# Kernel optimization log

Measured on AMD Instinct MI355X. Metric: run time of the kernel, lower is better.

The kernel has to match this reference:

```python
import jax, jax.numpy as jnp
import numpy as np

N_NODES = 50000
N_EDGES = 800000
IN_CH = 128
HID = 256
OUT_CH = 10
N_GRAPHS = 64


def setup_inputs() -> dict:
    key = jax.random.key(0)
    ks = jax.random.split(key, 16)
    s = 0.02
    inp = {
        "x": jax.random.normal(ks[0], (N_NODES, IN_CH), dtype=jnp.float32),
        "edge_index": jax.random.randint(ks[1], (2, N_EDGES), 0, N_NODES, dtype=jnp.int64),
        "batch": jnp.sort(jax.random.randint(ks[2], (N_NODES,), 0, N_GRAPHS, dtype=jnp.int64)),
        # SAGEConv params: out = lin_l(mean_agg) + lin_r(x_root); lin_l has bias, lin_r does not (PyG default)
        "W1l": jax.random.normal(ks[3], (HID, IN_CH), dtype=jnp.float32) * s,
        "b1": jnp.zeros((HID,), jnp.float32),
        "W1r": jax.random.normal(ks[4], (HID, IN_CH), dtype=jnp.float32) * s,
        "W2l": jax.random.normal(ks[5], (HID, HID), dtype=jnp.float32) * s,
        "b2": jnp.zeros((HID,), jnp.float32),
        "W2r": jax.random.normal(ks[6], (HID, HID), dtype=jnp.float32) * s,
        "W3l": jax.random.normal(ks[7], (HID, HID), dtype=jnp.float32) * s,
        "b3": jnp.zeros((HID,), jnp.float32),
        "W3r": jax.random.normal(ks[8], (HID, HID), dtype=jnp.float32) * s,
        "lin1_W": jax.random.normal(ks[9], (HID // 2, HID), dtype=jnp.float32) * s,
        "lin1_b": jnp.zeros((HID // 2,), jnp.float32),
        "lin2_W": jax.random.normal(ks[10], (OUT_CH, HID // 2), dtype=jnp.float32) * s,
        "lin2_b": jnp.zeros((OUT_CH,), jnp.float32),
    }
    return inp


def _sage_conv(x, src, dst, Wl, bl, Wr):
    # mean-aggregate neighbor features at destination nodes
    msg_sum = jax.ops.segment_sum(x[src], dst, num_segments=N_NODES)  # [N, d]
    deg = jax.ops.segment_sum(jnp.ones((src.shape[0],), x.dtype), dst, num_segments=N_NODES)
    agg = msg_sum / jnp.maximum(deg, 1.0)[:, None]
    return agg @ Wl.T + bl + x @ Wr.T


def reference(x, edge_index, batch, W1l, b1, W1r, W2l, b2, W2r, W3l, b3, W3r,
              lin1_W, lin1_b, lin2_W, lin2_b):
    src, dst = edge_index[0], edge_index[1]
    h = jax.nn.relu(_sage_conv(x, src, dst, W1l, b1, W1r))
    h = jax.nn.relu(_sage_conv(h, src, dst, W2l, b2, W2r))
    h = jax.nn.relu(_sage_conv(h, src, dst, W3l, b3, W3r))
    # global_mean_pool over batch vector
    pooled_sum = jax.ops.segment_sum(h, batch, num_segments=N_GRAPHS)  # [G, HID]
    counts = jax.ops.segment_sum(jnp.ones((h.shape[0],), h.dtype), batch, num_segments=N_GRAPHS)
    g = pooled_sum / jnp.maximum(counts, 1.0)[:, None]
    g = jax.nn.relu(g @ lin1_W.T + lin1_b)
    # dropout is identity in eval mode
    return g @ lin2_W.T + lin2_b
```

## Files before the change

kernel.cpp:

```cpp
#include <hip/hip_runtime.h>
#include <hip/hip_bf16.h>


#define HID 256
typedef unsigned short ushort_t;
typedef __bf16 bf16x8 __attribute__((ext_vector_type(8)));
typedef float  f32x4  __attribute__((ext_vector_type(4)));
typedef float  f32x2  __attribute__((ext_vector_type(2)));

__device__ __forceinline__ unsigned short f2bf(float f) {
    unsigned int u = __float_as_uint(f);
    unsigned int r = (u + 0x7fffu + ((u >> 16) & 1u)) >> 16;
    return (unsigned short)r;
}
__device__ __forceinline__ float bflo(unsigned int u) { return __uint_as_float(u << 16); }
__device__ __forceinline__ float bfhi(unsigned int u) { return __uint_as_float(u & 0xffff0000u); }
__device__ __forceinline__ unsigned int packbf(float a, float b) {
    return (unsigned int)f2bf(a) | ((unsigned int)f2bf(b) << 16);
}
__device__ __forceinline__ void gld16(const void* g, void* l) {
    __builtin_amdgcn_global_load_lds(
        (const __attribute__((address_space(1))) unsigned int*)g,
        (__attribute__((address_space(3))) unsigned int*)l, 16, 0, 0);
}
__device__ __forceinline__ void fma8(float* a, float w, const uint4 v) {
    a[0] = fmaf(w, bflo(v.x), a[0]); a[1] = fmaf(w, bfhi(v.x), a[1]);
    a[2] = fmaf(w, bflo(v.y), a[2]); a[3] = fmaf(w, bfhi(v.y), a[3]);
    a[4] = fmaf(w, bflo(v.z), a[4]); a[5] = fmaf(w, bfhi(v.z), a[5]);
    a[6] = fmaf(w, bflo(v.w), a[6]); a[7] = fmaf(w, bfhi(v.w), a[7]);
}
__device__ __forceinline__ void fma8_f8(float* a, float w, const uint2 v) {
    const f32x2 c01 = __builtin_amdgcn_cvt_pk_f32_fp8(v.x, false);
    const f32x2 c23 = __builtin_amdgcn_cvt_pk_f32_fp8(v.x, true);
    const f32x2 c45 = __builtin_amdgcn_cvt_pk_f32_fp8(v.y, false);
    const f32x2 c67 = __builtin_amdgcn_cvt_pk_f32_fp8(v.y, true);
    a[0] = fmaf(w, c01.x, a[0]); a[1] = fmaf(w, c01.y, a[1]);
    a[2] = fmaf(w, c23.x, a[2]); a[3] = fmaf(w, c23.y, a[3]);
    a[4] = fmaf(w, c45.x, a[4]); a[5] = fmaf(w, c45.y, a[5]);
    a[6] = fmaf(w, c67.x, a[6]); a[7] = fmaf(w, c67.y, a[7]);
}
__device__ __forceinline__ void acc8(float* a, const uint4 v) {
    a[0] += bflo(v.x); a[1] += bfhi(v.x);
    a[2] += bflo(v.y); a[3] += bfhi(v.y);
    a[4] += bflo(v.z); a[5] += bfhi(v.z);
    a[6] += bflo(v.w); a[7] += bfhi(v.w);
}
__device__ __forceinline__ int4 load4idx(const int* __restrict__ csr, int pbase, int e1m1) {
    int4 r;
    r.x = csr[min(pbase + 0, e1m1)];
    r.y = csr[min(pbase + 1, e1m1)];
    r.z = csr[min(pbase + 2, e1m1)];
    r.w = csr[min(pbase + 3, e1m1)];
    return r;
}

#define NBUCK 256
#define NPB_BUCK 196
#define BCAP 4096

__global__ __launch_bounds__(256)
void cvt_kernel(const float* __restrict__ x, ushort_t* __restrict__ xb, int nx4,
                const float* __restrict__ W1l, const float* __restrict__ W1r,
                const float* __restrict__ W2l, const float* __restrict__ W2r,
                const float* __restrict__ W3l, const float* __restrict__ W3r,
                ushort_t* __restrict__ wdst, int s1, int s2,
                int* __restrict__ bcursor) {
    const int t = blockIdx.x * 256 + threadIdx.x;
    if (t < NBUCK) bcursor[t] = 0;
    if (t < nx4) {
        const int i = t * 4;
        const float4 v = *(const float4*)(x + i);
        *(uint2*)(xb + i) = make_uint2(packbf(v.x, v.y), packbf(v.z, v.w));
        return;
    }
    int off = t - nx4;
    const int total = 2 * s1 + 4 * s2;
    if (off >= total) return;
    const int i = off;
    const float* src;
    if (off < s1) src = W1l;
    else if ((off -= s1) < s1) src = W1r;
    else if ((off -= s1) < s2) src = W2l;
    else if ((off -= s2) < s2) src = W2r;
    else if ((off -= s2) < s2) src = W3l;
    else { off -= s2; src = W3r; }
    wdst[i] = f2bf(src[off]);
}

__global__ __launch_bounds__(256)
void binA_kernel(const int* __restrict__ src, const int* __restrict__ dst,
                 int* __restrict__ bcursor, unsigned int* __restrict__ staging, int E) {
    __shared__ int hist[NBUCK];
    __shared__ int wbase[NBUCK];
    const int tid = threadIdx.x;
    hist[tid] = 0;
    __syncthreads();
    const int i0 = blockIdx.x * 2048;
    int d8[8], s8[8], b8[8];
    #pragma unroll
    for (int j = 0; j < 8; ++j) {
        const int i = i0 + j * 256 + tid;
        if (i < E) {
            d8[j] = dst[i];
            s8[j] = src[i];
            b8[j] = d8[j] / NPB_BUCK;
            atomicAdd(&hist[b8[j]], 1);
        } else b8[j] = -1;
    }
    __syncthreads();
    {
        const int b = tid;
        const int cnt = hist[b];
        int wb = 0;
        if (cnt > 0) wb = atomicAdd(&bcursor[b], cnt);
        wbase[b] = b * BCAP + wb;
        hist[b] = 0;
    }
    __syncthreads();
    #pragma unroll
    for (int j = 0; j < 8; ++j) {
        if (b8[j] >= 0) {
            const int pos = wbase[b8[j]] + atomicAdd(&hist[b8[j]], 1);
            if (pos < (b8[j] + 1) * BCAP)
                staging[pos] = ((unsigned int)(d8[j] - b8[j] * NPB_BUCK) << 16) | (unsigned int)s8[j];
        }
    }
}

__global__ __launch_bounds__(256)
void binB_kernel(const unsigned int* __restrict__ staging, const int* __restrict__ bcursor,
                 int* __restrict__ csr, int* __restrict__ offsets, int nn, int E) {
    __shared__ unsigned int sedge[BCAP];
    __shared__ int cnt[NBUCK];
    __shared__ int bsum[4];
    __shared__ int wt[4];
    const int b = blockIdx.x, tid = threadIdx.x;
    const int lane = tid & 63, wid = tid >> 6;

    int part = (tid < b) ? bcursor[tid] : 0;
    #pragma unroll
    for (int d = 1; d < 64; d <<= 1) part += __shfl_xor(part, d, 64);
    if (lane == 0) bsum[wid] = part;
    const int mycnt = min(bcursor[b], BCAP);
    __syncthreads();
    const int base = bsum[0] + bsum[1] + bsum[2] + bsum[3];

    for (int i = tid; i < mycnt; i += 256) sedge[i] = staging[b * BCAP + i];
    cnt[tid] = 0;
    __syncthreads();
    for (int i = tid; i < mycnt; i += 256) atomicAdd(&cnt[sedge[i] >> 16], 1);
    __syncthreads();

    const int v = cnt[tid];
    int incl = v;
    #pragma unroll
    for (int d = 1; d < 64; d <<= 1) {
        int t = __shfl_up(incl, d, 64);
        if (lane >= d) incl += t;
    }
    if (lane == 63) wt[wid] = incl;
    __syncthreads();
    int wb = 0;
    #pragma unroll
    for (int w = 0; w < 4; ++w) { int t = wt[w]; if (w < wid) wb += t; }
    const int excl = wb + incl - v;

    const int node = b * NPB_BUCK + tid;
    if (tid < NPB_BUCK && node < nn) offsets[node] = base + excl;
    if (b == NBUCK - 1 && tid == 0) offsets[nn] = E;
    __syncthreads();
    cnt[tid] = excl;
    __syncthreads();

    for (int i = tid; i < mycnt; i += 256) {
        const unsigned int e = sedge[i];
        const int p = atomicAdd(&cnt[e >> 16], 1);
        csr[base + p] = (int)(e & 0xFFFFu);
    }
}

template <int C>
__global__ __launch_bounds__(256)
void agg_kernel(const ushort_t* __restrict__ h, const int* __restrict__ offsets,
                const int* __restrict__ csr, ushort_t* __restrict__ out, int nn) {
    constexpr int CL = C / 8;
    constexpr int EW = 64 / CL;
    constexpr int RPE = 4 * EW;
    const int node = (blockIdx.x * 256 + threadIdx.x) >> 6;
    if (node >= nn) return;
    const int lane = threadIdx.x & 63;
    const int cl = lane & (CL - 1);
    const int eo = lane / CL;
    const int e0 = offsets[node], e1 = offsets[node + 1];
    const int deg = e1 - e0;
    const int rounds = (deg + RPE - 1) / RPE;
    const int e1m1 = max(e1 - 1, 0);
    float a[8] = {0.f, 0.f, 0.f, 0.f, 0.f, 0.f, 0.f, 0.f};
    int pb = e0 + eo * 4;
    if (rounds > 0) {
        int4 idx = load4idx(csr, pb, e1m1);
        for (int r2 = 0; r2 < rounds; ++r2) {
            const int4 cur = idx;
            const int pcur = pb;
            pb += RPE;
            if (r2 + 1 < rounds) idx = load4idx(csr, pb, e1m1);
            const uint4 v0 = *(const uint4*)(h + (size_t)cur.x * C + cl * 8);
            const uint4 v1 = *(const uint4*)(h + (size_t)cur.y * C + cl * 8);
            const uint4 v2 = *(const uint4*)(h + (size_t)cur.z * C + cl * 8);
            const uint4 v3 = *(const uint4*)(h + (size_t)cur.w * C + cl * 8);
            fma8(a, (pcur + 0 < e1) ? 1.f : 0.f, v0);
            fma8(a, (pcur + 1 < e1) ? 1.f : 0.f, v1);
            fma8(a, (pcur + 2 < e1) ? 1.f : 0.f, v2);
            fma8(a, (pcur + 3 < e1) ? 1.f : 0.f, v3);
        }
    }
    #pragma unroll
    for (int d = CL; d < 64; d <<= 1)
        #pragma unroll
        for (int r = 0; r < 8; ++r) a[r] += __shfl_xor(a[r], d, 64);
    if (eo == 0) {
        const float inv = 1.0f / fmaxf((float)deg, 1.0f);
        uint4 o;
        o.x = packbf(a[0] * inv, a[1] * inv);
        o.y = packbf(a[2] * inv, a[3] * inv);
        o.z = packbf(a[4] * inv, a[5] * inv);
        o.w = packbf(a[6] * inv, a[7] * inv);
        *(uint4*)(out + (size_t)node * C + cl * 8) = o;
    }
}

__global__ __launch_bounds__(256)
void agg8_kernel(const unsigned char* __restrict__ h8, const int* __restrict__ offsets,
                 const int* __restrict__ csr, ushort_t* __restrict__ out, int nn) {
    const int node = (blockIdx.x * 256 + threadIdx.x) >> 6;
    if (node >= nn) return;
    const int lane = threadIdx.x & 63;
    const int cl = lane & 31;
    const int eo = lane >> 5;
    const int e0 = offsets[node], e1 = offsets[node + 1];
    const int deg = e1 - e0;
    const int rounds = (deg + 7) / 8;
    const int e1m1 = max(e1 - 1, 0);
    float a[8] = {0.f, 0.f, 0.f, 0.f, 0.f, 0.f, 0.f, 0.f};
    int pb = e0 + eo * 4;
    if (rounds > 0) {
        int4 idx = load4idx(csr, pb, e1m1);
        for (int r2 = 0; r2 < rounds; ++r2) {
            const int4 cur = idx;
            const int pcur = pb;
            pb += 8;
            if (r2 + 1 < rounds) idx = load4idx(csr, pb, e1m1);
            const uint2 v0 = *(const uint2*)(h8 + (size_t)cur.x * 256 + cl * 8);
            const uint2 v1 = *(const uint2*)(h8 + (size_t)cur.y * 256 + cl * 8);
            const uint2 v2 = *(const uint2*)(h8 + (size_t)cur.z * 256 + cl * 8);
            const uint2 v3 = *(const uint2*)(h8 + (size_t)cur.w * 256 + cl * 8);
            fma8_f8(a, (pcur + 0 < e1) ? 1.f : 0.f, v0);
            fma8_f8(a, (pcur + 1 < e1) ? 1.f : 0.f, v1);
            fma8_f8(a, (pcur + 2 < e1) ? 1.f : 0.f, v2);
            fma8_f8(a, (pcur + 3 < e1) ? 1.f : 0.f, v3);
        }
    }
    #pragma unroll
    for (int r = 0; r < 8; ++r) a[r] += __shfl_xor(a[r], 32, 64);
    if (eo == 0) {
        const float inv = 1.0f / fmaxf((float)deg, 1.0f);
        uint4 o;
        o.x = packbf(a[0] * inv, a[1] * inv);
        o.y = packbf(a[2] * inv, a[3] * inv);
        o.z = packbf(a[4] * inv, a[5] * inv);
        o.w = packbf(a[6] * inv, a[7] * inv);
        *(uint4*)(out + (size_t)node * 256 + cl * 8) = o;
    }
}

template <int K, bool W8>
__global__ __launch_bounds__(256, 2)
void gemm2_mfma(const ushort_t* __restrict__ A1, const ushort_t* __restrict__ A2,
                const ushort_t* __restrict__ W1, const ushort_t* __restrict__ W2,
                const float* __restrict__ bias, ushort_t* __restrict__ Cout,
                unsigned char* __restrict__ H8, int M) {
    __shared__ ushort_t As[2 * 128 * 64];
    __shared__ ushort_t Bs[2 * 128 * 64];
    const int tid = threadIdx.x;
    const int row0 = blockIdx.x * 128, col0 = blockIdx.y * 128;
    const int wave = tid >> 6, lane = tid & 63;
    const int wm = (wave & 1) * 64, wn = (wave >> 1) * 64;
    const int l15 = lane & 15, quad = lane >> 4;
    constexpr int NCH = K / 128;

    f32x4 acc[4][4] = {};

    #pragma unroll
    for (int phase = 0; phase < 2; ++phase) {
        const ushort_t* __restrict__ A = phase ? A2 : A1;
        const ushort_t* __restrict__ W = phase ? W2 : W1;
        for (int kc = 0; kc < NCH; ++kc) {
            const int kt = kc * 128;
            __syncthreads();
            #pragma unroll
            for (int p = 0; p < 8; ++p) {
                const int slot = p * 256 + tid;
                const int g = slot >> 10;
                const int r = (slot >> 3) & 127;
                const int c = slot & 7;
                const int cg = c ^ (r & 7);
                int ar = row0 + r; if (ar >= M) ar = M - 1;
                gld16(A + (size_t)ar * K + kt + g * 64 + cg * 8, &As[slot * 8]);
            }
            #pragma unroll
            for (int p = 0; p < 8; ++p) {
                const int slot = p * 256 + tid;
                const int g = slot >> 10;
                const int r = (slot >> 3) & 127;
                const int c = slot & 7;
                const int cg = c ^ (r & 7);
                gld16(W + (size_t)(col0 + r) * K + kt + g * 64 + cg * 8, &Bs[slot * 8]);
            }
            __syncthreads();
            #pragma unroll
            for (int g = 0; g < 2; ++g) {
                #pragma unroll
                for (int ks = 0; ks < 2; ++ks) {
                    const int kq = ks * 4 + quad;
                    bf16x8 af[4], bfv[4];
                    #pragma unroll
                    for (int i = 0; i < 4; ++i) {
                        const int r = wm + i * 16 + l15;
                        const int cl = kq ^ (r & 7);
                        af[i] = *(const bf16x8*)&As[g * 8192 + r * 64 + cl * 8];
                    }
                    #pragma unroll
                    for (int j = 0; j < 4; ++j) {
                        const int r = wn + j * 16 + l15;
                        const int cl = kq ^ (r & 7);
                        bfv[j] = *(const bf16x8*)&Bs[g * 8192 + r * 64 + cl * 8];
                    }
                    #pragma unroll
                    for (int i = 0; i < 4; ++i)
                        #pragma unroll
                        for (int j = 0; j < 4; ++j)
                            acc[i][j] = __builtin_amdgcn_mfma_f32_16x16x32_bf16(
                                af[i], bfv[j], acc[i][j], 0, 0, 0);
                }
            }
        }
    }

    #pragma unroll
    for (int i = 0; i < 4; ++i) {
        const int mbase = row0 + wm + i * 16 + quad * 4;
        #pragma unroll
        for (int j = 0; j < 4; ++j) {
            const int n = col0 + wn + j * 16 + l15;
            const float b = bias[n];
            #pragma unroll
            for (int reg = 0; reg < 4; ++reg) {
                const int mr = mbase + reg;
                const float v = fmaxf(acc[i][j][reg] + b, 0.f);
                const float vp = __shfl_xor(v, 1, 64);
                if (!(l15 & 1) && mr < M)
                    *(unsigned int*)(Cout + (size_t)mr * 256 + n) = packbf(v, vp);
                if (W8) {
                    const int p2 = __builtin_amdgcn_cvt_pk_fp8_f32(v, vp, 0, false);
                    const int q2 = __shfl_xor(p2, 2, 64);
                    if ((l15 & 3) == 0 && mr < M)
                        *(unsigned int*)(H8 + (size_t)mr * 256 + n) =
                            ((unsigned int)p2 & 0xFFFFu) | ((unsigned int)q2 << 16);
                }
            }
        }
    }
}

__global__ __launch_bounds__(256)
void pool_mlp_kernel(const ushort_t* __restrict__ h, const int* __restrict__ batch, int nn,
                     const float* __restrict__ lin1W, const float* __restrict__ lin1b,
                     const float* __restrict__ lin2W, const float* __restrict__ lin2b,
                     float* __restrict__ out) {
    const int g = blockIdx.x;
    const int tid = threadIdx.x;
    int lo = 0, hi = nn;
    while (lo < hi) { int mid = (lo + hi) >> 1; if (batch[mid] < g) lo = mid + 1; else hi = mid; }
    const int s = lo;
    hi = nn;
    while (lo < hi) { int mid = (lo + hi) >> 1; if (batch[mid] < g + 1) lo = mid + 1; else hi = mid; }
    const int e = lo;

    const int cl = tid & 31, rg = tid >> 5;
    float a[8] = {0.f, 0.f, 0.f, 0.f, 0.f, 0.f, 0.f, 0.f};
    for (int n = s + rg; n < e; n += 8) {
        const uint4 v = *(const uint4*)(h + (size_t)n * 256 + cl * 8);
        acc8(a, v);
    }
    __shared__ float red[8][256];
    #pragma unroll
    for (int r = 0; r < 8; ++r) red[rg][cl * 8 + r] = a[r];
    __syncthreads();
    __shared__ float meanv[256];
    float ssum = 0.f;
    #pragma unroll
    for (int r = 0; r < 8; ++r) ssum += red[r][tid];
    meanv[tid] = ssum / fmaxf((float)(e - s), 1.0f);
    __syncthreads();
    __shared__ float g1[128];
    if (tid < 128) {
        float acc = lin1b[tid];
        #pragma unroll 4
        for (int k = 0; k < 256; k += 4) {
            const float4 w = *(const float4*)(lin1W + tid * 256 + k);
            acc += meanv[k] * w.x + meanv[k + 1] * w.y + meanv[k + 2] * w.z + meanv[k + 3] * w.w;
        }
        g1[tid] = fmaxf(acc, 0.f);
    }
    __syncthreads();
    if (tid < 10) {
        float o = lin2b[tid];
        #pragma unroll 4
        for (int k = 0; k < 128; k += 4) {
            const float4 w = *(const float4*)(lin2W + tid * 128 + k);
            o += g1[k] * w.x + g1[k + 1] * w.y + g1[k + 2] * w.z + g1[k + 3] * w.w;
        }
        out[g * 10 + tid] = o;
    }
}

extern "C" void kernel_launch(void* const* d_in, const int* in_sizes, int n_in,
                              void* d_out, int out_size, void* d_ws, size_t ws_size,
                              hipStream_t stream) {
    const float* x     = (const float*)d_in[0];
    const int*   eidx  = (const int*)d_in[1];
    const int*   batch = (const int*)d_in[2];
    const float* W1l = (const float*)d_in[3];
    const float* b1  = (const float*)d_in[4];
    const float* W1r = (const float*)d_in[5];
    const float* W2l = (const float*)d_in[6];
    const float* b2  = (const float*)d_in[7];
    const float* W2r = (const float*)d_in[8];
    const float* W3l = (const float*)d_in[9];
    const float* b3  = (const float*)d_in[10];
    const float* W3r = (const float*)d_in[11];
    const float* lin1W = (const float*)d_in[12];
    const float* lin1b = (const float*)d_in[13];
    const float* lin2W = (const float*)d_in[14];
    const float* lin2b = (const float*)d_in[15];
    float* out = (float*)d_out;

    const int E  = in_sizes[1] / 2;
    const int NN = in_sizes[2];
    const int IN = 128;
    const int* src = eidx;
    const int* dst = eidx + E;

    char* ws = (char*)d_ws;
    size_t off = 0;
    auto alloc = [&](size_t bytes) { void* p = ws + off; off += (bytes + 255) / 256 * 256; return p; };
    ushort_t* xb  = (ushort_t*)alloc((size_t)NN * IN * 2);
    ushort_t* agg = (ushort_t*)alloc((size_t)NN * HID * 2);
    ushort_t* hA  = (ushort_t*)alloc((size_t)NN * HID * 2);
    ushort_t* hB  = (ushort_t*)alloc((size_t)NN * HID * 2);
    unsigned char* h8 = (unsigned char*)alloc((size_t)NN * HID);
    const int s1 = HID * IN, s2 = HID * HID;
    ushort_t* wb  = (ushort_t*)alloc((size_t)(2 * s1 + 4 * s2) * 2);
    int* offsets   = (int*)alloc((size_t)(NN + 1) * 4);
    int* csr       = (int*)alloc((size_t)E * 4);
    unsigned int* staging = (unsigned int*)alloc((size_t)NBUCK * BCAP * 4);
    int* bcursor   = (int*)alloc(NBUCK * 4);
    (void)ws_size; (void)n_in; (void)out_size;

    const ushort_t* W1lb = wb;
    const ushort_t* W1rb = wb + s1;
    const ushort_t* W2lb = wb + 2 * s1;
    const ushort_t* W2rb = wb + 2 * s1 + s2;
    const ushort_t* W3lb = wb + 2 * s1 + 2 * s2;
    const ushort_t* W3rb = wb + 2 * s1 + 3 * s2;

    const int TB = 256;
    const int mgrid = (NN + 127) / 128;

    const int nx4 = NN * IN / 4;
    const int wtotal = 2 * s1 + 4 * s2;
    cvt_kernel<<<(nx4 + wtotal + TB - 1) / TB, TB, 0, stream>>>(
        x, xb, nx4, W1l, W1r, W2l, W2r, W3l, W3r, wb, s1, s2, bcursor);

    binA_kernel<<<(E + 2047) / 2048, TB, 0, stream>>>(src, dst, bcursor, staging, E);
    binB_kernel<<<NBUCK, TB, 0, stream>>>(staging, bcursor, csr, offsets, NN, E);

    agg_kernel<128><<<(NN + 3) / 4, TB, 0, stream>>>(xb, offsets, csr, agg, NN);
    gemm2_mfma<128, true><<<dim3(mgrid, 2), TB, 0, stream>>>(agg, xb, W1lb, W1rb, b1, hA, h8, NN);
    agg8_kernel<<<(NN + 3) / 4, TB, 0, stream>>>(h8, offsets, csr, agg, NN);
    gemm2_mfma<256, true><<<dim3(mgrid, 2), TB, 0, stream>>>(agg, hA, W2lb, W2rb, b2, hB, h8, NN);
    agg8_kernel<<<(NN + 3) / 4, TB, 0, stream>>>(h8, offsets, csr, agg, NN);
    gemm2_mfma<256, false><<<dim3(mgrid, 2), TB, 0, stream>>>(agg, hB, W3lb, W3rb, b3, hA, nullptr, NN);

    pool_mlp_kernel<<<64, TB, 0, stream>>>(hA, batch, NN, lin1W, lin1b, lin2W, lin2b, out);
}
```

Measured before the change: 354.3 us.

## Split global mean pool into many-block partial sums with atomics plus MLP kernel

```diff
diff --git a/kernel.cpp b/kernel.cpp
--- a/kernel.cpp
+++ b/kernel.cpp
@@ -39,12 +39,6 @@
     a[4] = fmaf(w, c45.x, a[4]); a[5] = fmaf(w, c45.y, a[5]);
     a[6] = fmaf(w, c67.x, a[6]); a[7] = fmaf(w, c67.y, a[7]);
 }
-__device__ __forceinline__ void acc8(float* a, const uint4 v) {
-    a[0] += bflo(v.x); a[1] += bfhi(v.x);
-    a[2] += bflo(v.y); a[3] += bfhi(v.y);
-    a[4] += bflo(v.z); a[5] += bfhi(v.z);
-    a[6] += bflo(v.w); a[7] += bfhi(v.w);
-}
 __device__ __forceinline__ int4 load4idx(const int* __restrict__ csr, int pbase, int e1m1) {
     int4 r;
     r.x = csr[min(pbase + 0, e1m1)];
@@ -64,9 +58,10 @@
                 const float* __restrict__ W2l, const float* __restrict__ W2r,
                 const float* __restrict__ W3l, const float* __restrict__ W3r,
                 ushort_t* __restrict__ wdst, int s1, int s2,
-                int* __restrict__ bcursor) {
+                int* __restrict__ bcursor, float* __restrict__ pooled) {
     const int t = blockIdx.x * 256 + threadIdx.x;
     if (t < NBUCK) bcursor[t] = 0;
+    if (t < 64 * 256 / 4) *(float4*)(pooled + t * 4) = make_float4(0.f, 0.f, 0.f, 0.f);
     if (t < nx4) {
         const int i = t * 4;
         const float4 v = *(const float4*)(x + i);
@@ -373,10 +368,42 @@
 }
 
 __global__ __launch_bounds__(256)
-void pool_mlp_kernel(const ushort_t* __restrict__ h, const int* __restrict__ batch, int nn,
-                     const float* __restrict__ lin1W, const float* __restrict__ lin1b,
-                     const float* __restrict__ lin2W, const float* __restrict__ lin2b,
-                     float* __restrict__ out) {
+void pool_partial_kernel(const ushort_t* __restrict__ h, const int* __restrict__ batch,
+                         float* __restrict__ pooled, int nn) {
+    const int n0 = blockIdx.x * 64;
+    if (n0 >= nn) return;
+    const int n1 = min(n0 + 64, nn);
+    const int tid = threadIdx.x;
+    const int cl = tid & 31, rg = tid >> 5;
+    const int g0 = batch[n0];
+    const int g1 = batch[n1 - 1];
+    float a0[8] = {0.f, 0.f, 0.f, 0.f, 0.f, 0.f, 0.f, 0.f};
+    float a1[8] = {0.f, 0.f, 0.f, 0.f, 0.f, 0.f, 0.f, 0.f};
+    for (int n = n0 + rg; n < n1; n += 8) {
+        const uint4 v = *(const uint4*)(h + (size_t)n * 256 + cl * 8);
+        const float w1 = (batch[n] != g0) ? 1.f : 0.f;
+        fma8(a0, 1.f - w1, v);
+        fma8(a1, w1, v);
+    }
+    __shared__ float red[8][512];
+    #pragma unroll
+    for (int r = 0; r < 8; ++r) {
+        red[rg][cl * 8 + r] = a0[r];
+        red[rg][256 + cl * 8 + r] = a1[r];
+    }
+    __syncthreads();
+    float s0 = 0.f, s1 = 0.f;
+    #pragma unroll
+    for (int r = 0; r < 8; ++r) { s0 += red[r][tid]; s1 += red[r][256 + tid]; }
+    atomicAdd(&pooled[g0 * 256 + tid], s0);
+    if (g1 != g0) atomicAdd(&pooled[g1 * 256 + tid], s1);
+}
+
+__global__ __launch_bounds__(256)
+void mlp_kernel(const float* __restrict__ pooled, const int* __restrict__ batch, int nn,
+                const float* __restrict__ lin1W, const float* __restrict__ lin1b,
+                const float* __restrict__ lin2W, const float* __restrict__ lin2b,
+                float* __restrict__ out) {
     const int g = blockIdx.x;
     const int tid = threadIdx.x;
     int lo = 0, hi = nn;
@@ -385,24 +412,10 @@
     hi = nn;
     while (lo < hi) { int mid = (lo + hi) >> 1; if (batch[mid] < g + 1) lo = mid + 1; else hi = mid; }
     const int e = lo;
-
-    const int cl = tid & 31, rg = tid >> 5;
-    float a[8] = {0.f, 0.f, 0.f, 0.f, 0.f, 0.f, 0.f, 0.f};
-    for (int n = s + rg; n < e; n += 8) {
-        const uint4 v = *(const uint4*)(h + (size_t)n * 256 + cl * 8);
-        acc8(a, v);
-    }
-    __shared__ float red[8][256];
-    #pragma unroll
-    for (int r = 0; r < 8; ++r) red[rg][cl * 8 + r] = a[r];
-    __syncthreads();
     __shared__ float meanv[256];
-    float ssum = 0.f;
-    #pragma unroll
-    for (int r = 0; r < 8; ++r) ssum += red[r][tid];
-    meanv[tid] = ssum / fmaxf((float)(e - s), 1.0f);
-    __syncthreads();
-    __shared__ float g1[128];
+    __shared__ float g1v[128];
+    meanv[tid] = pooled[g * 256 + tid] / fmaxf((float)(e - s), 1.0f);
+    __syncthreads();
     if (tid < 128) {
         float acc = lin1b[tid];
         #pragma unroll 4
@@ -410,7 +423,7 @@
             const float4 w = *(const float4*)(lin1W + tid * 256 + k);
             acc += meanv[k] * w.x + meanv[k + 1] * w.y + meanv[k + 2] * w.z + meanv[k + 3] * w.w;
         }
-        g1[tid] = fmaxf(acc, 0.f);
+        g1v[tid] = fmaxf(acc, 0.f);
     }
     __syncthreads();
     if (tid < 10) {
@@ -418,7 +431,7 @@
         #pragma unroll 4
         for (int k = 0; k < 128; k += 4) {
             const float4 w = *(const float4*)(lin2W + tid * 128 + k);
-            o += g1[k] * w.x + g1[k + 1] * w.y + g1[k + 2] * w.z + g1[k + 3] * w.w;
+            o += g1v[k] * w.x + g1v[k + 1] * w.y + g1v[k + 2] * w.z + g1v[k + 3] * w.w;
         }
         out[g * 10 + tid] = o;
     }
@@ -465,6 +478,7 @@
     int* csr       = (int*)alloc((size_t)E * 4);
     unsigned int* staging = (unsigned int*)alloc((size_t)NBUCK * BCAP * 4);
     int* bcursor   = (int*)alloc(NBUCK * 4);
+    float* pooled  = (float*)alloc(64 * 256 * 4);
     (void)ws_size; (void)n_in; (void)out_size;
 
     const ushort_t* W1lb = wb;
@@ -480,7 +494,7 @@
     const int nx4 = NN * IN / 4;
     const int wtotal = 2 * s1 + 4 * s2;
     cvt_kernel<<<(nx4 + wtotal + TB - 1) / TB, TB, 0, stream>>>(
-        x, xb, nx4, W1l, W1r, W2l, W2r, W3l, W3r, wb, s1, s2, bcursor);
+        x, xb, nx4, W1l, W1r, W2l, W2r, W3l, W3r, wb, s1, s2, bcursor, pooled);
 
     binA_kernel<<<(E + 2047) / 2048, TB, 0, stream>>>(src, dst, bcursor, staging, E);
     binB_kernel<<<NBUCK, TB, 0, stream>>>(staging, bcursor, csr, offsets, NN, E);
@@ -492,5 +506,6 @@
     agg8_kernel<<<(NN + 3) / 4, TB, 0, stream>>>(h8, offsets, csr, agg, NN);
     gemm2_mfma<256, false><<<dim3(mgrid, 2), TB, 0, stream>>>(agg, hB, W3lb, W3rb, b3, hA, nullptr, NN);
 
-    pool_mlp_kernel<<<64, TB, 0, stream>>>(hA, batch, NN, lin1W, lin1b, lin2W, lin2b, out);
-}
+    pool_partial_kernel<<<(NN + 63) / 64, TB, 0, stream>>>(hA, batch, pooled, NN);
+    mlp_kernel<<<64, TB, 0, stream>>>(pooled, batch, NN, lin1W, lin1b, lin2W, lin2b, out);
+}
```

After: 338.8 us. 1.05x faster.
